# Kernel optimization log

Measured on AMD Instinct MI355X. Metric: run time of the kernel, lower is better.

Reference implementation:

```python
import jax, jax.numpy as jnp
import numpy as np

BITS = 4
PACK = 32 // BITS  # 8 nibbles per int32
GROUPSIZE = 128
IN_F, OUT_F = 4096, 11008
N_GROUPS = IN_F // GROUPSIZE


def setup_inputs() -> dict:
    key = jax.random.key(0)
    k1, k2, k3, k4, k5 = jax.random.split(key, 5)
    x = jax.random.normal(k1, (8192, IN_F), dtype=jnp.float32)
    # packed int4 weights: 8 values per int32 along the infeatures axis
    qweight = jax.random.randint(k2, (IN_F // PACK, OUT_F), jnp.iinfo(jnp.int32).min,
                                 jnp.iinfo(jnp.int32).max, dtype=jnp.int32)
    # packed int4 zero points: 8 values per int32 along the outfeatures axis
    qzeros = jax.random.randint(k3, (N_GROUPS, OUT_F // PACK), jnp.iinfo(jnp.int32).min,
                                jnp.iinfo(jnp.int32).max, dtype=jnp.int32)
    # small positive per-group scales, as produced by GPTQ quantization
    scales = (jax.random.uniform(k4, (N_GROUPS, OUT_F), dtype=jnp.float32) * 0.01 + 0.001)
    g_idx = (jnp.arange(IN_F, dtype=jnp.int32) // GROUPSIZE).astype(jnp.int32)
    bias = jax.random.normal(k5, (OUT_F,), dtype=jnp.float32)
    return {"x": x, "qweight": qweight, "qzeros": qzeros, "scales": scales,
            "g_idx": g_idx, "bias": bias}


def _unpack_int4_rows(packed):
    # packed: [in/8, out] int32 -> [in, out] int32 nibbles
    shifts = (BITS * jnp.arange(PACK, dtype=jnp.int32))  # [8]
    nib = (packed[:, None, :] >> shifts[None, :, None]) & 0xF  # [in/8, 8, out]
    return nib.reshape(packed.shape[0] * PACK, packed.shape[1])


def _unpack_int4_cols(packed):
    # packed: [G, out/8] int32 -> [G, out] int32 nibbles
    shifts = (BITS * jnp.arange(PACK, dtype=jnp.int32))  # [8]
    nib = (packed[:, :, None] >> shifts[None, None, :]) & 0xF  # [G, out/8, 8]
    return nib.reshape(packed.shape[0], packed.shape[1] * PACK)


def reference(x, qweight, qzeros, scales, g_idx, bias):
    q = _unpack_int4_rows(qweight)            # [in, out] int4 values in [0,15]
    z = _unpack_int4_cols(qzeros) + 1         # pack() stored zeros-1; GPTQ dequant adds it back
    # per-input-channel group lookup via g_idx
    s = scales[g_idx]                         # [in, out]
    zf = z[g_idx].astype(jnp.float32)         # [in, out]
    w = (q.astype(jnp.float32) - zf) * s      # dequantized weight [in, out]
    out = jnp.matmul(x, w) + bias             # [tokens, out]
    return out
```

## Files before the change

kernel.cpp:

```cpp
#include <hip/hip_runtime.h>
#include <stdint.h>

#define TOKENS 8192
#define IN_F   4096
#define OUT_F  11008
#define GROUPSIZE 128

#define BM 256
#define BN 256
#define BK 64
#define NT  (IN_F / BK)
#define NBM (TOKENS / BM)
#define NBN (OUT_F / BN)
#define NWG (NBM * NBN)

typedef __attribute__((ext_vector_type(8)))  short          bf16x8;
typedef __attribute__((ext_vector_type(4)))  float          f32x4;
typedef __attribute__((ext_vector_type(8)))  unsigned short u16x8;
typedef __attribute__((ext_vector_type(16))) unsigned short u16x16;

static __device__ __forceinline__ unsigned short f2bf(float f) {
    union { float f; unsigned int u; } v; v.f = f;
    unsigned int u = v.u;
    u += 0x7fffu + ((u >> 16) & 1u);
    return (unsigned short)(u >> 16);
}

__global__ void cvt_x_kernel(const float* __restrict__ x,
                             unsigned short* __restrict__ xb) {
    int i = (blockIdx.x * 256 + threadIdx.x) * 8;
    const float4* p = (const float4*)(x + i);
    float4 a = p[0];
    float4 b = p[1];
    u16x8 o;
    o[0] = f2bf(a.x); o[1] = f2bf(a.y); o[2] = f2bf(a.z); o[3] = f2bf(a.w);
    o[4] = f2bf(b.x); o[5] = f2bf(b.y); o[6] = f2bf(b.z); o[7] = f2bf(b.w);
    *(u16x8*)(xb + i) = o;
}

__global__ void dequant_kernel(const int* __restrict__ qweight,
                               const int* __restrict__ qzeros,
                               const float* __restrict__ scales,
                               unsigned short* __restrict__ Wt) {
    const int t  = threadIdx.x;
    const int n  = blockIdx.x * 256 + t;
    const int g  = blockIdx.y;
    const float s  = scales[g * OUT_F + n];
    const int   zq = ((qzeros[g * (OUT_F / 8) + (n >> 3)] >> (4 * (n & 7))) & 0xF) + 1;
    const float zs = (float)zq * s;

    const int* qrow = qweight + (size_t)(g * 16) * OUT_F + n;
    unsigned short* wrow = Wt + (size_t)n * IN_F + g * GROUPSIZE;

    int qw[16];
#pragma unroll
    for (int r = 0; r < 16; ++r)
        qw[r] = qrow[(size_t)r * OUT_F];

#pragma unroll
    for (int r = 0; r < 16; r += 2) {
        u16x16 o;
#pragma unroll
        for (int j = 0; j < 8; ++j) {
            o[j]     = f2bf(fmaf((float)((qw[r]     >> (4 * j)) & 0xF), s, -zs));
            o[j + 8] = f2bf(fmaf((float)((qw[r + 1] >> (4 * j)) & 0xF), s, -zs));
        }
        *(u16x16*)(wrow + r * 8) = o;
    }
}

#define GLD16(gp, lp)                                                        \
    __builtin_amdgcn_global_load_lds(                                        \
        (const __attribute__((address_space(1))) unsigned int*)(gp),         \
        (__attribute__((address_space(3))) unsigned int*)(lp), 16, 0, 0)

#define BARRIER() do {                                                       \
    asm volatile("" ::: "memory");                                           \
    __builtin_amdgcn_s_barrier();                                            \
    asm volatile("" ::: "memory");                                           \
} while (0)

#define LGKM0() do {                                                         \
    asm volatile("s_waitcnt lgkmcnt(0)" ::: "memory");                       \
    __builtin_amdgcn_sched_barrier(0);                                       \
} while (0)

__global__ __launch_bounds__(512, 2) void gemm_bias_kernel(
    const unsigned short* __restrict__ A,
    const unsigned short* __restrict__ Bt,
    const float* __restrict__ bias,
    float* __restrict__ C) {
    extern __shared__ char smem_c[];

    const int tid = threadIdx.x;
    const int l   = tid & 63;
    const int w   = tid >> 6;
    const int wr  = w >> 2;
    const int wc  = w & 3;

    const int bid = blockIdx.x;
    const int swz = (bid & 7) * (NWG / 8) + (bid >> 3);
    const int m0  = (swz / NBN) * BM;
    const int n0  = (swz % NBN) * BN;

    const int sperm = ((l & 7) ^ (l >> 3)) * 8;
    const unsigned short* aG = A  + (size_t)(m0 + w * 16 + (l >> 3)) * IN_F + sperm;
    const unsigned short* bG = Bt + (size_t)(n0 + w * 16 + (l >> 3)) * IN_F + sperm;
    char* sA = smem_c + w * 2048 + l * 16;
    char* sB = sA + 32768;

#define STAGE_A(b, h, tt) do {                                               \
    GLD16(aG + (size_t)((h) * 128    ) * IN_F + (tt) * 64,                   \
          sA + (b) * 65536 + (h) * 16384);                                   \
    GLD16(aG + (size_t)((h) * 128 + 8) * IN_F + (tt) * 64,                   \
          sA + (b) * 65536 + (h) * 16384 + 1024);                            \
} while (0)
#define STAGE_B(b, h, tt) do {                                               \
    GLD16(bG + (size_t)((h) * 128    ) * IN_F + (tt) * 64,                   \
          sB + (b) * 65536 + (h) * 16384);                                   \
    GLD16(bG + (size_t)((h) * 128 + 8) * IN_F + (tt) * 64,                   \
          sB + (b) * 65536 + (h) * 16384 + 1024);                            \
} while (0)

    const unsigned short* LAe = (const unsigned short*)smem_c;
    const unsigned short* LBe = (const unsigned short*)(smem_c + 32768);
    const int c0   = (((l >> 4) ^ (l & 7)) * 8);
    const int c1   = c0 ^ 32;
    const int arow = (wr * 128 + (l & 15)) * 64;
    const int brow = (wc * 64  + (l & 15)) * 64;

    f32x4  acc[8][4] = {};
    bf16x8 a0[2], a1[2], bfr[4][2];

#define RDA_PAIR(p, mi) do {                                                 \
    a0[0] = *(const bf16x8*)&(p)[arow + (mi) * 1024 + c0];                   \
    a0[1] = *(const bf16x8*)&(p)[arow + (mi) * 1024 + c1];                   \
    a1[0] = *(const bf16x8*)&(p)[arow + ((mi) + 1) * 1024 + c0];             \
    a1[1] = *(const bf16x8*)&(p)[arow + ((mi) + 1) * 1024 + c1];             \
} while (0)
#define RDB(p, nj) do {                                                      \
    bfr[nj][0] = *(const bf16x8*)&(p)[brow + (nj) * 1024 + c0];              \
    bfr[nj][1] = *(const bf16x8*)&(p)[brow + (nj) * 1024 + c1];              \
} while (0)
#define MM0(mi, nj, ks)                                                      \
    acc[mi][nj] = __builtin_amdgcn_mfma_f32_16x16x32_bf16(                   \
        a0[ks], bfr[nj][ks], acc[mi][nj], 0, 0, 0)
#define MM1(mi, nj, ks)                                                      \
    acc[mi][nj] = __builtin_amdgcn_mfma_f32_16x16x32_bf16(                   \
        a1[ks], bfr[nj][ks], acc[mi][nj], 0, 0, 0)
#define QUADP(e) do {                                                        \
    __builtin_amdgcn_s_setprio(1);                                           \
    MM0(e,0,0); MM0(e,1,0); MM0(e,2,0); MM0(e,3,0);                          \
    MM1((e)+1,0,0); MM1((e)+1,1,0); MM1((e)+1,2,0); MM1((e)+1,3,0);          \
    MM0(e,0,1); MM0(e,1,1); MM0(e,2,1); MM0(e,3,1);                          \
    MM1((e)+1,0,1); MM1((e)+1,1,1); MM1((e)+1,2,1); MM1((e)+1,3,1);          \
    __builtin_amdgcn_s_setprio(0);                                           \
} while (0)

    STAGE_A(0, 0, 0); STAGE_A(0, 1, 0);
    STAGE_B(0, 0, 0); STAGE_B(0, 1, 0);
    STAGE_B(1, 0, 1); STAGE_B(1, 1, 1);
    asm volatile("s_waitcnt vmcnt(4)" ::: "memory");
    __builtin_amdgcn_sched_barrier(0);
    BARRIER();

    for (int t = 0; t < NT; ++t) {
        const int bt = t & 1;
        const int bo = bt ^ 1;
        const unsigned short* pA = LAe + bt * 32768;
        const unsigned short* pB = LBe + bt * 32768;

        RDB(pB, 0); RDB(pB, 1); RDB(pB, 2); RDB(pB, 3);
        RDA_PAIR(pA, 0);
        if (t + 1 < NT) STAGE_A(bo, 0, t + 1);
        BARRIER();
        LGKM0();
        QUADP(0);
        BARRIER();

        RDA_PAIR(pA, 2);
        if (t + 1 < NT) STAGE_A(bo, 1, t + 1);
        BARRIER();
        LGKM0();
        QUADP(2);
        BARRIER();

        RDA_PAIR(pA, 4);
        if (t + 2 < NT) STAGE_B(bt, 0, t + 2);
        BARRIER();
        LGKM0();
        QUADP(4);
        BARRIER();

        RDA_PAIR(pA, 6);
        if (t + 2 < NT) STAGE_B(bt, 1, t + 2);
        BARRIER();
        LGKM0();
        QUADP(6);
        if (t < NT - 2)
            asm volatile("s_waitcnt vmcnt(4)" ::: "memory");
        else if (t == NT - 2)
            asm volatile("s_waitcnt vmcnt(0)" ::: "memory");
        __builtin_amdgcn_sched_barrier(0);
        BARRIER();
    }

    const int col = l & 15;
    const int r0  = (l >> 4) * 4;
#pragma unroll
    for (int nj = 0; nj < 4; ++nj) {
        const int n = n0 + wc * 64 + nj * 16 + col;
        const float bv = bias[n];
#pragma unroll
        for (int mi = 0; mi < 8; ++mi) {
            const int m = m0 + wr * 128 + mi * 16 + r0;
#pragma unroll
            for (int r = 0; r < 4; ++r)
                C[(size_t)(m + r) * OUT_F + n] = acc[mi][nj][r] + bv;
        }
    }
}

__global__ __launch_bounds__(256) void fallback_kernel(
    const float* __restrict__ x, const int* __restrict__ qweight,
    const int* __restrict__ qzeros, const float* __restrict__ scales,
    const float* __restrict__ bias, float* __restrict__ C) {
    const int n = blockIdx.x * 16 + (threadIdx.x & 15);
    const int m = blockIdx.y * 16 + (threadIdx.x >> 4);
    float acc = 0.f;
    const float* xr = x + (size_t)m * IN_F;
    for (int g = 0; g < IN_F / GROUPSIZE; ++g) {
        const float s  = scales[g * OUT_F + n];
        const float zs = s * (float)(((qzeros[g * (OUT_F / 8) + (n >> 3)]
                                       >> (4 * (n & 7))) & 0xF) + 1);
        for (int kp = g * 16; kp < g * 16 + 16; ++kp) {
            const int qw = qweight[kp * OUT_F + n];
#pragma unroll
            for (int j = 0; j < 8; ++j) {
                const float w = fmaf((float)((qw >> (4 * j)) & 0xF), s, -zs);
                acc = fmaf(xr[kp * 8 + j], w, acc);
            }
        }
    }
    C[(size_t)m * OUT_F + n] = acc + bias[n];
}

extern "C" void kernel_launch(void* const* d_in, const int* in_sizes, int n_in,
                              void* d_out, int out_size, void* d_ws, size_t ws_size,
                              hipStream_t stream) {
    const float* x       = (const float*)d_in[0];
    const int*   qweight = (const int*)  d_in[1];
    const int*   qzeros  = (const int*)  d_in[2];
    const float* scales  = (const float*)d_in[3];
    const float* bias    = (const float*)d_in[5];
    float* out = (float*)d_out;

    const size_t xb_bytes = (size_t)TOKENS * IN_F * sizeof(unsigned short);
    const size_t wt_bytes = (size_t)OUT_F  * IN_F * sizeof(unsigned short);

    if (ws_size >= xb_bytes + wt_bytes) {
        static bool attr_done = false;
        if (!attr_done) {
            (void)hipFuncSetAttribute((const void*)gemm_bias_kernel,
                                      hipFuncAttributeMaxDynamicSharedMemorySize,
                                      131072);
            attr_done = true;
        }
        unsigned short* xb = (unsigned short*)d_ws;
        unsigned short* Wt = (unsigned short*)((char*)d_ws + xb_bytes);
        cvt_x_kernel<<<(TOKENS * IN_F) / (256 * 8), 256, 0, stream>>>(x, xb);
        dequant_kernel<<<dim3(OUT_F / 256, IN_F / GROUPSIZE), 256, 0, stream>>>(
            qweight, qzeros, scales, Wt);
        gemm_bias_kernel<<<NWG, 512, 131072, stream>>>(xb, Wt, bias, out);
    } else {
        fallback_kernel<<<dim3(OUT_F / 16, TOKENS / 16), 256, 0, stream>>>(
            x, qweight, qzeros, scales, bias, out);
    }
}
```

Baseline: 1.089 ms.

## Merge conversion and dequant into one launch and remap GEMM tiles per XCD

The separate x-to-bf16 conversion and weight dequant kernels become a single prep kernel that picks its branch from the block index, removing one launch and the gap between kernels. The GEMM tile mapping also changes: each of the 8 XCDs now owns 4 consecutive M tiles and walks across N tiles, replacing the earlier interleaved swizzle. The aim is better L2 reuse of A rows inside each XCD, in exchange for a different pattern of B reuse.

Result: no change. 1.098 ms (+0.8%).

```diff
diff --git a/kernel.cpp b/kernel.cpp
--- a/kernel.cpp
+++ b/kernel.cpp
@@ -14,6 +14,9 @@
 #define NBN (OUT_F / BN)
 #define NWG (NBM * NBN)
 
+#define CVT_BLOCKS ((TOKENS * IN_F) / (256 * 8))
+#define DEQ_BLOCKS ((OUT_F / 256) * (IN_F / GROUPSIZE))
+
 typedef __attribute__((ext_vector_type(8)))  short          bf16x8;
 typedef __attribute__((ext_vector_type(4)))  float          f32x4;
 typedef __attribute__((ext_vector_type(8)))  unsigned short u16x8;
@@ -26,46 +29,46 @@
     return (unsigned short)(u >> 16);
 }
 
-__global__ void cvt_x_kernel(const float* __restrict__ x,
-                             unsigned short* __restrict__ xb) {
-    int i = (blockIdx.x * 256 + threadIdx.x) * 8;
-    const float4* p = (const float4*)(x + i);
-    float4 a = p[0];
-    float4 b = p[1];
-    u16x8 o;
-    o[0] = f2bf(a.x); o[1] = f2bf(a.y); o[2] = f2bf(a.z); o[3] = f2bf(a.w);
-    o[4] = f2bf(b.x); o[5] = f2bf(b.y); o[6] = f2bf(b.z); o[7] = f2bf(b.w);
-    *(u16x8*)(xb + i) = o;
-}
-
-__global__ void dequant_kernel(const int* __restrict__ qweight,
-                               const int* __restrict__ qzeros,
-                               const float* __restrict__ scales,
-                               unsigned short* __restrict__ Wt) {
-    const int t  = threadIdx.x;
-    const int n  = blockIdx.x * 256 + t;
-    const int g  = blockIdx.y;
-    const float s  = scales[g * OUT_F + n];
-    const int   zq = ((qzeros[g * (OUT_F / 8) + (n >> 3)] >> (4 * (n & 7))) & 0xF) + 1;
-    const float zs = (float)zq * s;
-
-    const int* qrow = qweight + (size_t)(g * 16) * OUT_F + n;
-    unsigned short* wrow = Wt + (size_t)n * IN_F + g * GROUPSIZE;
-
-    int qw[16];
-#pragma unroll
-    for (int r = 0; r < 16; ++r)
-        qw[r] = qrow[(size_t)r * OUT_F];
-
-#pragma unroll
-    for (int r = 0; r < 16; r += 2) {
-        u16x16 o;
-#pragma unroll
-        for (int j = 0; j < 8; ++j) {
-            o[j]     = f2bf(fmaf((float)((qw[r]     >> (4 * j)) & 0xF), s, -zs));
-            o[j + 8] = f2bf(fmaf((float)((qw[r + 1] >> (4 * j)) & 0xF), s, -zs));
-        }
-        *(u16x16*)(wrow + r * 8) = o;
+__global__ __launch_bounds__(256) void prep_kernel(
+    const float* __restrict__ x, unsigned short* __restrict__ xb,
+    const int* __restrict__ qweight, const int* __restrict__ qzeros,
+    const float* __restrict__ scales, unsigned short* __restrict__ Wt) {
+    const int t = threadIdx.x;
+    if (blockIdx.x < CVT_BLOCKS) {
+        int i = (blockIdx.x * 256 + t) * 8;
+        const float4* p = (const float4*)(x + i);
+        float4 a = p[0];
+        float4 b = p[1];
+        u16x8 o;
+        o[0] = f2bf(a.x); o[1] = f2bf(a.y); o[2] = f2bf(a.z); o[3] = f2bf(a.w);
+        o[4] = f2bf(b.x); o[5] = f2bf(b.y); o[6] = f2bf(b.z); o[7] = f2bf(b.w);
+        *(u16x8*)(xb + i) = o;
+    } else {
+        const int b  = blockIdx.x - CVT_BLOCKS;
+        const int n  = (b % (OUT_F / 256)) * 256 + t;
+        const int g  = b / (OUT_F / 256);
+        const float s  = scales[g * OUT_F + n];
+        const int   zq = ((qzeros[g * (OUT_F / 8) + (n >> 3)] >> (4 * (n & 7))) & 0xF) + 1;
+        const float zs = (float)zq * s;
+
+        const int* qrow = qweight + (size_t)(g * 16) * OUT_F + n;
+        unsigned short* wrow = Wt + (size_t)n * IN_F + g * GROUPSIZE;
+
+        int qw[16];
+#pragma unroll
+        for (int r = 0; r < 16; ++r)
+            qw[r] = qrow[(size_t)r * OUT_F];
+
+#pragma unroll
+        for (int r = 0; r < 16; r += 2) {
+            u16x16 o;
+#pragma unroll
+            for (int j = 0; j < 8; ++j) {
+                o[j]     = f2bf(fmaf((float)((qw[r]     >> (4 * j)) & 0xF), s, -zs));
+                o[j + 8] = f2bf(fmaf((float)((qw[r + 1] >> (4 * j)) & 0xF), s, -zs));
+            }
+            *(u16x16*)(wrow + r * 8) = o;
+        }
     }
 }
 
@@ -98,10 +101,11 @@
     const int wr  = w >> 2;
     const int wc  = w & 3;
 
-    const int bid = blockIdx.x;
-    const int swz = (bid & 7) * (NWG / 8) + (bid >> 3);
-    const int m0  = (swz / NBN) * BM;
-    const int n0  = (swz % NBN) * BN;
+    const int bid  = blockIdx.x;
+    const int xcd  = bid & 7;
+    const int q    = bid >> 3;
+    const int m0   = (xcd * 4 + (q & 3)) * BM;
+    const int n0   = (q >> 2) * BN;
 
     const int sperm = ((l & 7) ^ (l >> 3)) * 8;
     const unsigned short* aG = A  + (size_t)(m0 + w * 16 + (l >> 3)) * IN_F + sperm;
@@ -268,9 +272,8 @@
         }
         unsigned short* xb = (unsigned short*)d_ws;
         unsigned short* Wt = (unsigned short*)((char*)d_ws + xb_bytes);
-        cvt_x_kernel<<<(TOKENS * IN_F) / (256 * 8), 256, 0, stream>>>(x, xb);
-        dequant_kernel<<<dim3(OUT_F / 256, IN_F / GROUPSIZE), 256, 0, stream>>>(
-            qweight, qzeros, scales, Wt);
+        prep_kernel<<<CVT_BLOCKS + DEQ_BLOCKS, 256, 0, stream>>>(
+            x, xb, qweight, qzeros, scales, Wt);
         gemm_bias_kernel<<<NWG, 512, 131072, stream>>>(xb, Wt, bias, out);
     } else {
         fallback_kernel<<<dim3(OUT_F / 16, TOKENS / 16), 256, 0, stream>>>(
```
